# Optimization experiments

Measured on AMD Instinct MI355X. Metric: run time of the kernel, lower is better.

## Reference

```python
import jax, jax.numpy as jnp
import numpy as np

K_TOP = 32
ALPHA = 1.0


def setup_inputs() -> dict:
    key = jax.random.key(0)
    k1, k2, k3 = jax.random.split(key, 3)
    x = jax.random.normal(k1, (1, 512, 1024), dtype=jnp.float32)
    keys = jax.random.normal(k2, (200000, 1024), dtype=jnp.float32) * 0.02
    vals = jax.random.normal(k3, (200000, 1024), dtype=jnp.float32)
    return {"x": x, "keys": keys, "vals": vals}


def reference(x, keys, vals):
    B, L, D = x.shape
    q = x.reshape(B * L, D)                       # [N, D]
    scores = q @ keys.T                           # [N, num_slots] dense matmul
    topv, topi = jax.lax.top_k(scores, K_TOP)     # [N, k]
    attn = jax.nn.softmax(topv, axis=-1)          # [N, k]
    sel_vals = vals[topi]                         # [N, k, D] gather
    out = jnp.einsum('nk,nkd->nd', attn, sel_vals)
    return ALPHA * out.reshape(B, L, D)
```

## Files before the change

### kernel.cpp

```cpp
#include <hip/hip_runtime.h>
#include <hip/hip_bf16.h>
#include <stdint.h>


#define KTOP 32
#define MROWS 512
#define NKEYS 200000
#define DDIM 1024

#define BM 128
#define BN 128
#define BK 64
#define LDT 72
#define NCOLT 1563
#define NT 1568
#define TCAP 256
#define CCAP 256
#define TMARGIN 0.125f

typedef __attribute__((ext_vector_type(4))) float f32x4;
typedef __attribute__((ext_vector_type(8))) short short8;

__device__ __forceinline__ unsigned short f2bf(float f) {
    __hip_bfloat16 h = __float2bfloat16(f);
    return *reinterpret_cast<unsigned short*>(&h);
}
__device__ __forceinline__ int enc16(unsigned short u) {
    return (int)(u ^ ((u & 0x8000u) ? 0xFFFFu : 0x8000u));
}
__device__ __forceinline__ float dec_enc(int e) {
    unsigned short u = (unsigned short)((e & 0x8000) ? (e ^ 0x8000) : (e ^ 0xFFFF));
    return __uint_as_float((unsigned int)u << 16);
}
__device__ __forceinline__ float bf2f(unsigned short u) {
    return __uint_as_float((unsigned int)u << 16);
}

__global__ void cvt_x_kernel(const float* __restrict__ x, unsigned short* __restrict__ xb) {
    int i = blockIdx.x * blockDim.x + threadIdx.x;
    f32x4 v = reinterpret_cast<const f32x4*>(x)[i];
    ushort4 o;
    o.x = f2bf(v.x); o.y = f2bf(v.y); o.z = f2bf(v.z); o.w = f2bf(v.w);
    reinterpret_cast<ushort4*>(xb)[i] = o;
}

__global__ __launch_bounds__(256, 3)
void score_gemm(const float* __restrict__ keys, const unsigned short* __restrict__ xb,
                unsigned short* __restrict__ scores, unsigned short* __restrict__ tilemax) {
    __shared__ unsigned short As[BM * LDT];
    __shared__ unsigned short Bs[BN * LDT];
    __shared__ int tmax[BM];

    const int tid  = threadIdx.x;
    const int lane = tid & 63;
    const int wid  = tid >> 6;
    const int wr   = wid >> 1;
    const int wc   = wid & 1;

    const int bid = blockIdx.x;
    const int s   = bid & 7;
    const int u   = bid >> 3;
    const int rt  = u & 3;
    const int g   = (u >> 2) * 8 + s;
    if (g >= NCOLT) return;
    const int row0 = rt * BM;
    const int col0 = g * BN;

    if (tid < BM) tmax[tid] = 0;

    f32x4 acc[4][4];
#pragma unroll
    for (int m = 0; m < 4; m++)
#pragma unroll
        for (int n = 0; n < 4; n++) acc[m][n] = (f32x4){0.f, 0.f, 0.f, 0.f};

    short8 areg[4];
    f32x4  breg[8];

    auto loadA = [&](int k0) {
#pragma unroll
        for (int i = 0; i < 4; i++) {
            int c = i * 256 + tid;
            int r = c >> 3, j = c & 7;
            areg[i] = *reinterpret_cast<const short8*>(xb + (size_t)(row0 + r) * DDIM + k0 + j * 8);
        }
    };
    auto loadB = [&](int k0) {
#pragma unroll
        for (int i = 0; i < 8; i++) {
            int c = i * 256 + tid;
            int r = c >> 4, j = c & 15;
            int gr = col0 + r; gr = (gr < NKEYS) ? gr : (NKEYS - 1);
            breg[i] = *reinterpret_cast<const f32x4*>(keys + (size_t)gr * DDIM + k0 + j * 4);
        }
    };
    auto writeLDS = [&]() {
#pragma unroll
        for (int i = 0; i < 4; i++) {
            int c = i * 256 + tid;
            int r = c >> 3, j = c & 7;
            *reinterpret_cast<short8*>(&As[r * LDT + j * 8]) = areg[i];
        }
#pragma unroll
        for (int i = 0; i < 8; i++) {
            int c = i * 256 + tid;
            int r = c >> 4, j = c & 15;
            ushort4 o;
            o.x = f2bf(breg[i].x); o.y = f2bf(breg[i].y);
            o.z = f2bf(breg[i].z); o.w = f2bf(breg[i].w);
            *reinterpret_cast<ushort4*>(&Bs[r * LDT + j * 4]) = o;
        }
    };

    const int rl = lane & 15;
    const int kl = (lane >> 4) * 8;

    auto compute = [&]() {
        const unsigned short* Ab = &As[(wr * 64 + rl) * LDT + kl];
        const unsigned short* Bb = &Bs[(wc * 64 + rl) * LDT + kl];
#pragma unroll
        for (int kk = 0; kk < BK; kk += 32) {
            short8 af[4], bf[4];
#pragma unroll
            for (int m = 0; m < 4; m++) af[m] = *reinterpret_cast<const short8*>(Ab + m * 16 * LDT + kk);
#pragma unroll
            for (int n = 0; n < 4; n++) bf[n] = *reinterpret_cast<const short8*>(Bb + n * 16 * LDT + kk);
#pragma unroll
            for (int m = 0; m < 4; m++)
#pragma unroll
                for (int n = 0; n < 4; n++)
                    acc[m][n] = __builtin_amdgcn_mfma_f32_16x16x32_bf16(af[m], bf[n], acc[m][n], 0, 0, 0);
        }
    };

    loadA(0); loadB(0);
    for (int t = 0; t < DDIM / BK; t++) {
        __syncthreads();
        writeLDS();
        __syncthreads();
        if (t + 1 < DDIM / BK) { loadA((t + 1) * BK); loadB((t + 1) * BK); }
        compute();
    }

    const int rg = lane >> 4;
#pragma unroll
    for (int m = 0; m < 4; m++) {
#pragma unroll
        for (int j = 0; j < 4; j++) {
            int lrow = wr * 64 + m * 16 + rg * 4 + j;
            int grow = row0 + lrow;
            float mx = -1e30f;
#pragma unroll
            for (int n = 0; n < 4; n++) {
                float v = acc[m][n][j];
                mx = fmaxf(mx, v);
                int gcol = col0 + wc * 64 + n * 16 + rl;
                if (gcol < NKEYS)
                    scores[(size_t)grow * NKEYS + gcol] = f2bf(v);
            }
#pragma unroll
            for (int sft = 1; sft < 16; sft <<= 1) mx = fmaxf(mx, __shfl_xor(mx, sft));
            if (rl == 0)
                atomicMax(&tmax[lrow], enc16(f2bf(mx)));
        }
    }
    __syncthreads();
    if (tid < BM)
        tilemax[(size_t)(row0 + tid) * NT + g] = (unsigned short)tmax[tid];
}

__global__ __launch_bounds__(256)
void select_kernel(const float* __restrict__ x, const float* __restrict__ keys,
                   const float* __restrict__ vals, const unsigned short* __restrict__ scores,
                   const unsigned short* __restrict__ tilemax, float* __restrict__ out) {
    const int n    = blockIdx.x;
    const int tid  = threadIdx.x;
    const int lane = tid & 63;
    const int w    = tid >> 6;

    __shared__ __align__(16) float qs[DDIM];
    __shared__ unsigned short enc_t[NT];
    __shared__ int    hist[256];
    __shared__ int    tiles[TCAP];
    __shared__ int    cand[CCAP];
    __shared__ double rsc[CCAP];
    __shared__ float  wgt[KTOP];
    __shared__ int    topslot[KTOP];
    __shared__ float  topval[KTOP];
    __shared__ int    ntiles, ncand, sbsel, sabove, st32e;

    reinterpret_cast<f32x4*>(qs)[tid] = reinterpret_cast<const f32x4*>(x + (size_t)n * DDIM)[tid];
    hist[tid] = 0;
    if (tid < 32) { wgt[tid] = 0.f; topslot[tid] = -1; }
    if (tid == 0) { ntiles = 0; ncand = 0; }
    for (int i = tid; i < NT; i += 256)
        enc_t[i] = (i < NCOLT) ? tilemax[(size_t)n * NT + i] : 0;
    __syncthreads();

    for (int i = tid; i < NT; i += 256) atomicAdd(&hist[enc_t[i] >> 8], 1);
    __syncthreads();
    if (tid == 0) {
        int cum = 0, b = 255;
        for (; b >= 0; b--) { cum += hist[b]; if (cum >= KTOP) break; }
        sbsel = b; sabove = cum - hist[b];
    }
    __syncthreads();
    const int bsel = sbsel;
    hist[tid] = 0;
    __syncthreads();
    for (int i = tid; i < NT; i += 256) {
        int e = enc_t[i];
        if ((e >> 8) == bsel) atomicAdd(&hist[e & 0xFF], 1);
    }
    __syncthreads();
    if (tid == 0) {
        int cum = sabove, lb = 255;
        for (; lb >= 0; lb--) { cum += hist[lb]; if (cum >= KTOP) break; }
        st32e = (bsel << 8) | lb;
    }
    __syncthreads();
    const float thr = dec_enc(st32e) - TMARGIN;

    for (int i = tid; i < NT; i += 256) {
        if (dec_enc(enc_t[i]) >= thr) {
            int p = atomicAdd(&ntiles, 1);
            if (p < TCAP) tiles[p] = i;
        }
    }
    __syncthreads();
    const int nt = ntiles < TCAP ? ntiles : TCAP;

    for (int idx = tid; idx < nt * BN; idx += 256) {
        int col = tiles[idx >> 7] * BN + (idx & 127);
        if (col < NKEYS) {
            float v = bf2f(scores[(size_t)n * NKEYS + col]);
            if (v >= thr) {
                int p = atomicAdd(&ncand, 1);
                if (p < CCAP) cand[p] = col;
            }
        }
    }
    __syncthreads();
    const int cnt = ncand < CCAP ? ncand : CCAP;

    for (int ci = w; ci < cnt; ci += 4) {
        const f32x4* kv = reinterpret_cast<const f32x4*>(keys + (size_t)cand[ci] * DDIM) + lane * 4;
        const f32x4* qv = reinterpret_cast<const f32x4*>(qs) + lane * 4;
        double a = 0.0;
#pragma unroll
        for (int i = 0; i < 4; i++) {
            f32x4 q = qv[i], k = kv[i];
            a += (double)q.x * k.x + (double)q.y * k.y + (double)q.z * k.z + (double)q.w * k.w;
        }
#pragma unroll
        for (int sft = 32; sft >= 1; sft >>= 1) a += __shfl_xor(a, sft);
        if (lane == 0) rsc[ci] = a;
    }
    __syncthreads();

    if (w == 0) {
        double v0[4]; int id0[4];
#pragma unroll
        for (int sft = 0; sft < 4; sft++) {
            int p = lane + sft * 64;
            if (p < cnt) { v0[sft] = rsc[p]; id0[sft] = p; } else { v0[sft] = -1e300; id0[sft] = -1; }
        }
        for (int k = 0; k < KTOP; k++) {
            double bv = v0[0]; int bi = id0[0];
#pragma unroll
            for (int sft = 1; sft < 4; sft++) if (v0[sft] > bv) { bv = v0[sft]; bi = id0[sft]; }
#pragma unroll
            for (int sft = 32; sft >= 1; sft >>= 1) {
                double ov = __shfl_xor(bv, sft);
                int    oi = __shfl_xor(bi, sft);
                if (ov > bv) { bv = ov; bi = oi; }
            }
            if (lane == 0) { topslot[k] = bi; topval[k] = (float)bv; }
#pragma unroll
            for (int sft = 0; sft < 4; sft++) if (bi >= 0 && id0[sft] == bi) v0[sft] = -1e300;
        }
    }
    __syncthreads();

    if (tid == 0) {
        float mx = topval[0];
        float sum = 0.f;
        for (int k = 0; k < KTOP; k++) {
            float e = (topslot[k] >= 0) ? expf(topval[k] - mx) : 0.f;
            wgt[k] = e; sum += e;
        }
        float inv = 1.f / sum;
        for (int k = 0; k < KTOP; k++) wgt[k] *= inv;
    }
    __syncthreads();

    f32x4 accv = (f32x4){0.f, 0.f, 0.f, 0.f};
    for (int k = 0; k < KTOP; k++) {
        int sl = topslot[k];
        if (sl >= 0) {
            float wk = wgt[k];
            f32x4 v = reinterpret_cast<const f32x4*>(vals + (size_t)cand[sl] * DDIM)[tid];
            accv.x += wk * v.x; accv.y += wk * v.y; accv.z += wk * v.z; accv.w += wk * v.w;
        }
    }
    reinterpret_cast<f32x4*>(out + (size_t)n * DDIM)[tid] = accv;
}

extern "C" void kernel_launch(void* const* d_in, const int* in_sizes, int n_in,
                              void* d_out, int out_size, void* d_ws, size_t ws_size,
                              hipStream_t stream) {
    const float* x    = (const float*)d_in[0];
    const float* keys = (const float*)d_in[1];
    const float* vals = (const float*)d_in[2];
    float* out = (float*)d_out;

    char* ws = (char*)d_ws;
    unsigned short* scores  = (unsigned short*)ws;
    unsigned short* xb      = (unsigned short*)(ws + 204800000);
    unsigned short* tilemax = (unsigned short*)(ws + 204800000 + 1048576);

    cvt_x_kernel<<<512, 256, 0, stream>>>(x, xb);
    score_gemm<<<4 * NT, 256, 0, stream>>>(keys, xb, scores, tilemax);
    select_kernel<<<MROWS, 256, 0, stream>>>(x, keys, vals, scores, tilemax, out);
}
```

Baseline: 475.5 us.

## Stream fp32 keys into LDS via async global_load_lds with triple buffering

The score GEMM now copies fp32 key tiles straight into a triple-buffered, XOR-swizzled LDS area using global_load_lds, and double-buffers the bf16 query tile. It replaces the register-staged load/convert/store plus two barriers per step with a software pipeline that waits on explicit vmcnt counts. The bf16 conversion moves into the compute loop, so each wave converts the B fragments it reads from LDS. LDS use roughly doubles (fp32 B, three copies), and the occupancy hint of 3 is dropped, so fewer blocks may fit per CU. The conversion work is also repeated across waves.

```diff
diff --git a/kernel.cpp b/kernel.cpp
--- a/kernel.cpp
+++ b/kernel.cpp
@@ -12,6 +12,7 @@
 #define BN 128
 #define BK 64
 #define LDT 72
+#define NSTEP 16
 #define NCOLT 1563
 #define NT 1568
 #define TCAP 256
@@ -44,11 +45,11 @@
     reinterpret_cast<ushort4*>(xb)[i] = o;
 }
 
-__global__ __launch_bounds__(256, 3)
+__global__ __launch_bounds__(256)
 void score_gemm(const float* __restrict__ keys, const unsigned short* __restrict__ xb,
                 unsigned short* __restrict__ scores, unsigned short* __restrict__ tilemax) {
-    __shared__ unsigned short As[BM * LDT];
-    __shared__ unsigned short Bs[BN * LDT];
+    __shared__ __align__(16) unsigned short As[2][BM * LDT];
+    __shared__ __align__(16) float Bsf[3][BN * BK];
     __shared__ int tmax[BM];
 
     const int tid  = threadIdx.x;
@@ -74,57 +75,71 @@
 #pragma unroll
         for (int n = 0; n < 4; n++) acc[m][n] = (f32x4){0.f, 0.f, 0.f, 0.f};
 
-    short8 areg[4];
-    f32x4  breg[8];
-
-    auto loadA = [&](int k0) {
+    short8 areg0[4], areg1[4];
+
+    auto loadA = [&](short8 (&ar)[4], int t) {
+        if (t >= NSTEP) return;
+        const int k0 = t * BK;
 #pragma unroll
         for (int i = 0; i < 4; i++) {
             int c = i * 256 + tid;
             int r = c >> 3, j = c & 7;
-            areg[i] = *reinterpret_cast<const short8*>(xb + (size_t)(row0 + r) * DDIM + k0 + j * 8);
+            ar[i] = *reinterpret_cast<const short8*>(xb + (size_t)(row0 + r) * DDIM + k0 + j * 8);
         }
     };
-    auto loadB = [&](int k0) {
-#pragma unroll
-        for (int i = 0; i < 8; i++) {
-            int c = i * 256 + tid;
-            int r = c >> 4, j = c & 15;
-            int gr = col0 + r; gr = (gr < NKEYS) ? gr : (NKEYS - 1);
-            breg[i] = *reinterpret_cast<const f32x4*>(keys + (size_t)gr * DDIM + k0 + j * 4);
-        }
-    };
-    auto writeLDS = [&]() {
+    auto writeA = [&](int asel, short8 (&ar)[4]) {
 #pragma unroll
         for (int i = 0; i < 4; i++) {
             int c = i * 256 + tid;
             int r = c >> 3, j = c & 7;
-            *reinterpret_cast<short8*>(&As[r * LDT + j * 8]) = areg[i];
-        }
+            *reinterpret_cast<short8*>(&As[asel][r * LDT + j * 8]) = ar[i];
+        }
+    };
+    auto issueB = [&](int t) {
+        if (t >= NSTEP) return;
+        const int bsel = t % 3;
+        const size_t kbyte = (size_t)t * 256;
+        char* ldsbase = (char*)&Bsf[bsel][0];
 #pragma unroll
         for (int i = 0; i < 8; i++) {
-            int c = i * 256 + tid;
-            int r = c >> 4, j = c & 15;
-            ushort4 o;
-            o.x = f2bf(breg[i].x); o.y = f2bf(breg[i].y);
-            o.z = f2bf(breg[i].z); o.w = f2bf(breg[i].w);
-            *reinterpret_cast<ushort4*>(&Bs[r * LDT + j * 4]) = o;
+            int cb = i * 256 + tid;
+            int r = cb >> 4, jc = cb & 15;
+            int js = jc ^ (r & 7);
+            int gr = col0 + r; gr = (gr < NKEYS) ? gr : (NKEYS - 1);
+            const char* src = (const char*)keys + (size_t)gr * 4096 + kbyte + (size_t)js * 16;
+            __builtin_amdgcn_global_load_lds(
+                (const __attribute__((address_space(1))) unsigned int*)src,
+                (__attribute__((address_space(3))) unsigned int*)(ldsbase + (size_t)cb * 16),
+                16, 0, 0);
         }
     };
 
     const int rl = lane & 15;
     const int kl = (lane >> 4) * 8;
 
-    auto compute = [&]() {
-        const unsigned short* Ab = &As[(wr * 64 + rl) * LDT + kl];
-        const unsigned short* Bb = &Bs[(wc * 64 + rl) * LDT + kl];
+    auto compute = [&](int asel, int bsel) {
+        const unsigned short* Ab = &As[asel][(wr * 64 + rl) * LDT + kl];
+        const float* Bf = &Bsf[bsel][0];
+        const int rB0 = wc * 64 + rl;
 #pragma unroll
         for (int kk = 0; kk < BK; kk += 32) {
             short8 af[4], bf[4];
 #pragma unroll
             for (int m = 0; m < 4; m++) af[m] = *reinterpret_cast<const short8*>(Ab + m * 16 * LDT + kk);
 #pragma unroll
-            for (int n = 0; n < 4; n++) bf[n] = *reinterpret_cast<const short8*>(Bb + n * 16 * LDT + kk);
+            for (int n = 0; n < 4; n++) {
+                int row = rB0 + n * 16;
+                int sw  = row & 7;
+                int jc0 = (kk + kl) >> 2;
+                f32x4 c0 = *reinterpret_cast<const f32x4*>(Bf + row * 64 + ((jc0 ^ sw) << 2));
+                f32x4 c1 = *reinterpret_cast<const f32x4*>(Bf + row * 64 + (((jc0 + 1) ^ sw) << 2));
+                short8 b;
+                b[0] = (short)f2bf(c0.x); b[1] = (short)f2bf(c0.y);
+                b[2] = (short)f2bf(c0.z); b[3] = (short)f2bf(c0.w);
+                b[4] = (short)f2bf(c1.x); b[5] = (short)f2bf(c1.y);
+                b[6] = (short)f2bf(c1.z); b[7] = (short)f2bf(c1.w);
+                bf[n] = b;
+            }
 #pragma unroll
             for (int m = 0; m < 4; m++)
 #pragma unroll
@@ -133,14 +148,37 @@
         }
     };
 
-    loadA(0); loadB(0);
-    for (int t = 0; t < DDIM / BK; t++) {
-        __syncthreads();
-        writeLDS();
-        __syncthreads();
-        if (t + 1 < DDIM / BK) { loadA((t + 1) * BK); loadB((t + 1) * BK); }
-        compute();
-    }
+#define SYNC(N) do { asm volatile("s_waitcnt vmcnt(" #N ")" ::: "memory");  \
+                     asm volatile("s_waitcnt lgkmcnt(0)" ::: "memory");     \
+                     __builtin_amdgcn_sched_barrier(0);                     \
+                     __builtin_amdgcn_s_barrier();                          \
+                     __builtin_amdgcn_sched_barrier(0); } while (0)
+
+    loadA(areg0, 0);
+    issueB(0); issueB(1);
+    loadA(areg1, 1);
+    writeA(0, areg0);
+    loadA(areg0, 2);
+    SYNC(16);
+
+    for (int t = 0; t < 12; t += 2) {
+        issueB(t + 2); writeA(1, areg1); loadA(areg1, t + 3);
+        compute(0, t % 3);
+        SYNC(16);
+        issueB(t + 3); writeA(0, areg0); loadA(areg0, t + 4);
+        compute(1, (t + 1) % 3);
+        SYNC(16);
+    }
+    issueB(14); writeA(1, areg1); loadA(areg1, 15);
+    compute(0, 0);
+    SYNC(16);
+    issueB(15); writeA(0, areg0);
+    compute(1, 1);
+    SYNC(12);
+    writeA(1, areg1);
+    compute(0, 2);
+    SYNC(0);
+    compute(1, 0);
 
     const int rg = lane >> 4;
 #pragma unroll
@@ -167,6 +205,7 @@
     __syncthreads();
     if (tid < BM)
         tilemax[(size_t)(row0 + tid) * NT + g] = (unsigned short)tmax[tid];
+#undef SYNC
 }
 
 __global__ __launch_bounds__(256)
```

New measurement: 881.2 us. 85.3% more time.

## Double-buffer score GEMM with direct global-to-LDS loads and swizzled layout

Applied to the files above, without the earlier changes.

Replaces the register-staged global loads and LDS write-back in the score GEMM with direct global-to-LDS async loads into a double-buffered, XOR-swizzled shared memory layout. The K tile drops to 32, and there is one barrier per step instead of two. Keys are now kept as fp32 in LDS and converted to bf16 at fragment-load time. The aim is to overlap memory traffic with MFMA work and remove register and VALU staging, at the cost of more LDS bytes for B and repeated bf16 conversion per wave. Correctness depends on the barrier also waiting for the async LDS loads to finish.

```diff
diff --git a/kernel.cpp b/kernel.cpp
--- a/kernel.cpp
+++ b/kernel.cpp
@@ -10,8 +10,8 @@
 
 #define BM 128
 #define BN 128
-#define BK 64
-#define LDT 72
+#define BK 32
+#define NSTEP 32
 #define NCOLT 1563
 #define NT 1568
 #define TCAP 256
@@ -47,8 +47,8 @@
 __global__ __launch_bounds__(256, 3)
 void score_gemm(const float* __restrict__ keys, const unsigned short* __restrict__ xb,
                 unsigned short* __restrict__ scores, unsigned short* __restrict__ tilemax) {
-    __shared__ unsigned short As[BM * LDT];
-    __shared__ unsigned short Bs[BN * LDT];
+    __shared__ __align__(16) unsigned short As[2][BM * BK];
+    __shared__ __align__(16) float          Bs[2][BN * BK];
     __shared__ int tmax[BM];
 
     const int tid  = threadIdx.x;
@@ -74,74 +74,76 @@
 #pragma unroll
         for (int n = 0; n < 4; n++) acc[m][n] = (f32x4){0.f, 0.f, 0.f, 0.f};
 
-    short8 areg[4];
-    f32x4  breg[8];
-
-    auto loadA = [&](int k0) {
+    auto issueAB = [&](int t, int b) {
+        char* abase = (char*)&As[b][0];
+        char* bbase = (char*)&Bs[b][0];
+#pragma unroll
+        for (int i = 0; i < 2; i++) {
+            int ca = i * 256 + tid;
+            int r = ca >> 2, jc = ca & 3;
+            int js = jc ^ ((r >> 1) & 3);
+            const char* src = (const char*)xb + (size_t)(row0 + r) * 2048 + (size_t)t * 64 + (size_t)js * 16;
+            __builtin_amdgcn_global_load_lds(
+                (const __attribute__((address_space(1))) unsigned int*)src,
+                (__attribute__((address_space(3))) unsigned int*)(abase + (size_t)ca * 16),
+                16, 0, 0);
+        }
 #pragma unroll
         for (int i = 0; i < 4; i++) {
-            int c = i * 256 + tid;
-            int r = c >> 3, j = c & 7;
-            areg[i] = *reinterpret_cast<const short8*>(xb + (size_t)(row0 + r) * DDIM + k0 + j * 8);
+            int cb = i * 256 + tid;
+            int r = cb >> 3, jc = cb & 7;
+            int js = jc ^ (r & 7);
+            int gr = col0 + r; gr = (gr < NKEYS) ? gr : (NKEYS - 1);
+            const char* src = (const char*)keys + (size_t)gr * 4096 + (size_t)t * 128 + (size_t)js * 16;
+            __builtin_amdgcn_global_load_lds(
+                (const __attribute__((address_space(1))) unsigned int*)src,
+                (__attribute__((address_space(3))) unsigned int*)(bbase + (size_t)cb * 16),
+                16, 0, 0);
         }
     };
-    auto loadB = [&](int k0) {
-#pragma unroll
-        for (int i = 0; i < 8; i++) {
-            int c = i * 256 + tid;
-            int r = c >> 4, j = c & 15;
-            int gr = col0 + r; gr = (gr < NKEYS) ? gr : (NKEYS - 1);
-            breg[i] = *reinterpret_cast<const f32x4*>(keys + (size_t)gr * DDIM + k0 + j * 4);
-        }
+
+    const int rl = lane & 15;
+    const int kg = lane >> 4;
+
+    auto compute = [&](int b) {
+        const unsigned short* Ab = &As[b][0];
+        const float* Bf = &Bs[b][0];
+        short8 af[4], bf[4];
+#pragma unroll
+        for (int m = 0; m < 4; m++) {
+            int ra = wr * 64 + m * 16 + rl;
+            int ja = kg ^ ((ra >> 1) & 3);
+            af[m] = *reinterpret_cast<const short8*>(Ab + ra * 32 + ja * 8);
+        }
+#pragma unroll
+        for (int n = 0; n < 4; n++) {
+            int rb = wc * 64 + n * 16 + rl;
+            int sw = rb & 7;
+            int jc0 = kg * 2;
+            f32x4 c0 = *reinterpret_cast<const f32x4*>(Bf + rb * 32 + ((jc0 ^ sw) << 2));
+            f32x4 c1 = *reinterpret_cast<const f32x4*>(Bf + rb * 32 + (((jc0 + 1) ^ sw) << 2));
+            short8 bq;
+            bq[0] = (short)f2bf(c0.x); bq[1] = (short)f2bf(c0.y);
+            bq[2] = (short)f2bf(c0.z); bq[3] = (short)f2bf(c0.w);
+            bq[4] = (short)f2bf(c1.x); bq[5] = (short)f2bf(c1.y);
+            bq[6] = (short)f2bf(c1.z); bq[7] = (short)f2bf(c1.w);
+            bf[n] = bq;
+        }
+#pragma unroll
+        for (int m = 0; m < 4; m++)
+#pragma unroll
+            for (int n = 0; n < 4; n++)
+                acc[m][n] = __builtin_amdgcn_mfma_f32_16x16x32_bf16(af[m], bf[n], acc[m][n], 0, 0, 0);
     };
-    auto writeLDS = [&]() {
-#pragma unroll
-        for (int i = 0; i < 4; i++) {
-            int c = i * 256 + tid;
-            int r = c >> 3, j = c & 7;
-            *reinterpret_cast<short8*>(&As[r * LDT + j * 8]) = areg[i];
-        }
-#pragma unroll
-        for (int i = 0; i < 8; i++) {
-            int c = i * 256 + tid;
-            int r = c >> 4, j = c & 15;
-            ushort4 o;
-            o.x = f2bf(breg[i].x); o.y = f2bf(breg[i].y);
-            o.z = f2bf(breg[i].z); o.w = f2bf(breg[i].w);
-            *reinterpret_cast<ushort4*>(&Bs[r * LDT + j * 4]) = o;
-        }
-    };
-
-    const int rl = lane & 15;
-    const int kl = (lane >> 4) * 8;
-
-    auto compute = [&]() {
-        const unsigned short* Ab = &As[(wr * 64 + rl) * LDT + kl];
-        const unsigned short* Bb = &Bs[(wc * 64 + rl) * LDT + kl];
-#pragma unroll
-        for (int kk = 0; kk < BK; kk += 32) {
-            short8 af[4], bf[4];
-#pragma unroll
-            for (int m = 0; m < 4; m++) af[m] = *reinterpret_cast<const short8*>(Ab + m * 16 * LDT + kk);
-#pragma unroll
-            for (int n = 0; n < 4; n++) bf[n] = *reinterpret_cast<const short8*>(Bb + n * 16 * LDT + kk);
-#pragma unroll
-            for (int m = 0; m < 4; m++)
-#pragma unroll
-                for (int n = 0; n < 4; n++)
-                    acc[m][n] = __builtin_amdgcn_mfma_f32_16x16x32_bf16(af[m], bf[n], acc[m][n], 0, 0, 0);
-        }
-    };
-
-    loadA(0); loadB(0);
-    for (int t = 0; t < DDIM / BK; t++) {
+
+    issueAB(0, 0);
+    for (int t = 0; t < NSTEP; t++) {
         __syncthreads();
-        writeLDS();
-        __syncthreads();
-        if (t + 1 < DDIM / BK) { loadA((t + 1) * BK); loadB((t + 1) * BK); }
-        compute();
-    }
-
+        if (t + 1 < NSTEP) issueAB(t + 1, (t + 1) & 1);
+        compute(t & 1);
+    }
+
+    __syncthreads();
     const int rg = lane >> 4;
 #pragma unroll
     for (int m = 0; m < 4; m++) {
```

After: 661.6 us. 39.1% more time.

## Restructure score GEMM so each block covers all query rows over 64 keys

Applied to the files above, without the earlier changes.

The score GEMM now uses 1024-thread blocks that each hold all 512 query rows in LDS and process a 64-key column tile. This removes the 4x re-read and re-conversion of fp32 keys that came from splitting the rows into four 128-row tiles. Tile maxima become per-64-key, so the select kernel scans twice as many tiles with a larger tile cap but reads finer-grained candidate tiles. The trade-offs are large LDS use per block (about 74KB), which limits occupancy, and a smaller per-wave MFMA tile (32x64), which lowers compute density.

```diff
diff --git a/kernel.cpp b/kernel.cpp
--- a/kernel.cpp
+++ b/kernel.cpp
@@ -8,13 +8,13 @@
 #define NKEYS 200000
 #define DDIM 1024
 
-#define BM 128
-#define BN 128
+#define BN2 64
 #define BK 64
 #define LDT 72
-#define NCOLT 1563
-#define NT 1568
-#define TCAP 256
+#define NSTEP 16
+#define NCOLT2 3125
+#define NT2 3136
+#define TCAP 512
 #define CCAP 256
 #define TMARGIN 0.125f
 
@@ -44,70 +44,55 @@
     reinterpret_cast<ushort4*>(xb)[i] = o;
 }
 
-__global__ __launch_bounds__(256, 3)
+__global__ __launch_bounds__(1024, 4)
 void score_gemm(const float* __restrict__ keys, const unsigned short* __restrict__ xb,
                 unsigned short* __restrict__ scores, unsigned short* __restrict__ tilemax) {
-    __shared__ unsigned short As[BM * LDT];
-    __shared__ unsigned short Bs[BN * LDT];
-    __shared__ int tmax[BM];
+    __shared__ unsigned short As[MROWS * LDT];
+    __shared__ unsigned short Bs[BN2 * LDT];
+    __shared__ int tmax[MROWS];
 
     const int tid  = threadIdx.x;
     const int lane = tid & 63;
-    const int wid  = tid >> 6;
-    const int wr   = wid >> 1;
-    const int wc   = wid & 1;
-
-    const int bid = blockIdx.x;
-    const int s   = bid & 7;
-    const int u   = bid >> 3;
-    const int rt  = u & 3;
-    const int g   = (u >> 2) * 8 + s;
-    if (g >= NCOLT) return;
-    const int row0 = rt * BM;
-    const int col0 = g * BN;
-
-    if (tid < BM) tmax[tid] = 0;
-
-    f32x4 acc[4][4];
-#pragma unroll
-    for (int m = 0; m < 4; m++)
+    const int w    = tid >> 6;
+
+    const int g    = blockIdx.x;
+    const int col0 = g * BN2;
+
+    if (tid < MROWS) tmax[tid] = 0;
+
+    f32x4 acc[2][4];
+#pragma unroll
+    for (int m = 0; m < 2; m++)
 #pragma unroll
         for (int n = 0; n < 4; n++) acc[m][n] = (f32x4){0.f, 0.f, 0.f, 0.f};
 
     short8 areg[4];
-    f32x4  breg[8];
+    f32x4  breg;
 
     auto loadA = [&](int k0) {
 #pragma unroll
         for (int i = 0; i < 4; i++) {
-            int c = i * 256 + tid;
+            int c = i * 1024 + tid;
             int r = c >> 3, j = c & 7;
-            areg[i] = *reinterpret_cast<const short8*>(xb + (size_t)(row0 + r) * DDIM + k0 + j * 8);
+            areg[i] = *reinterpret_cast<const short8*>(xb + (size_t)r * DDIM + k0 + j * 8);
         }
     };
     auto loadB = [&](int k0) {
-#pragma unroll
-        for (int i = 0; i < 8; i++) {
-            int c = i * 256 + tid;
-            int r = c >> 4, j = c & 15;
-            int gr = col0 + r; gr = (gr < NKEYS) ? gr : (NKEYS - 1);
-            breg[i] = *reinterpret_cast<const f32x4*>(keys + (size_t)gr * DDIM + k0 + j * 4);
-        }
+        int r = tid >> 4, j = tid & 15;
+        breg = *reinterpret_cast<const f32x4*>(keys + (size_t)(col0 + r) * DDIM + k0 + j * 4);
     };
     auto writeLDS = [&]() {
 #pragma unroll
         for (int i = 0; i < 4; i++) {
-            int c = i * 256 + tid;
+            int c = i * 1024 + tid;
             int r = c >> 3, j = c & 7;
             *reinterpret_cast<short8*>(&As[r * LDT + j * 8]) = areg[i];
         }
-#pragma unroll
-        for (int i = 0; i < 8; i++) {
-            int c = i * 256 + tid;
-            int r = c >> 4, j = c & 15;
+        {
+            int r = tid >> 4, j = tid & 15;
             ushort4 o;
-            o.x = f2bf(breg[i].x); o.y = f2bf(breg[i].y);
-            o.z = f2bf(breg[i].z); o.w = f2bf(breg[i].w);
+            o.x = f2bf(breg.x); o.y = f2bf(breg.y);
+            o.z = f2bf(breg.z); o.w = f2bf(breg.w);
             *reinterpret_cast<ushort4*>(&Bs[r * LDT + j * 4]) = o;
         }
     };
@@ -116,17 +101,17 @@
     const int kl = (lane >> 4) * 8;
 
     auto compute = [&]() {
-        const unsigned short* Ab = &As[(wr * 64 + rl) * LDT + kl];
-        const unsigned short* Bb = &Bs[(wc * 64 + rl) * LDT + kl];
+        const unsigned short* Ab = &As[(w * 32 + rl) * LDT + kl];
+        const unsigned short* Bb = &Bs[rl * LDT + kl];
 #pragma unroll
         for (int kk = 0; kk < BK; kk += 32) {
-            short8 af[4], bf[4];
-#pragma unroll
-            for (int m = 0; m < 4; m++) af[m] = *reinterpret_cast<const short8*>(Ab + m * 16 * LDT + kk);
+            short8 af[2], bf[4];
+#pragma unroll
+            for (int m = 0; m < 2; m++) af[m] = *reinterpret_cast<const short8*>(Ab + m * 16 * LDT + kk);
 #pragma unroll
             for (int n = 0; n < 4; n++) bf[n] = *reinterpret_cast<const short8*>(Bb + n * 16 * LDT + kk);
 #pragma unroll
-            for (int m = 0; m < 4; m++)
+            for (int m = 0; m < 2; m++)
 #pragma unroll
                 for (int n = 0; n < 4; n++)
                     acc[m][n] = __builtin_amdgcn_mfma_f32_16x16x32_bf16(af[m], bf[n], acc[m][n], 0, 0, 0);
@@ -134,29 +119,26 @@
     };
 
     loadA(0); loadB(0);
-    for (int t = 0; t < DDIM / BK; t++) {
+    for (int t = 0; t < NSTEP; t++) {
         __syncthreads();
         writeLDS();
         __syncthreads();
-        if (t + 1 < DDIM / BK) { loadA((t + 1) * BK); loadB((t + 1) * BK); }
+        if (t + 1 < NSTEP) { loadA((t + 1) * BK); loadB((t + 1) * BK); }
         compute();
     }
 
     const int rg = lane >> 4;
 #pragma unroll
-    for (int m = 0; m < 4; m++) {
+    for (int m = 0; m < 2; m++) {
 #pragma unroll
         for (int j = 0; j < 4; j++) {
-            int lrow = wr * 64 + m * 16 + rg * 4 + j;
-            int grow = row0 + lrow;
+            int lrow = w * 32 + m * 16 + rg * 4 + j;
             float mx = -1e30f;
 #pragma unroll
             for (int n = 0; n < 4; n++) {
                 float v = acc[m][n][j];
                 mx = fmaxf(mx, v);
-                int gcol = col0 + wc * 64 + n * 16 + rl;
-                if (gcol < NKEYS)
-                    scores[(size_t)grow * NKEYS + gcol] = f2bf(v);
+                scores[(size_t)lrow * NKEYS + col0 + n * 16 + rl] = f2bf(v);
             }
 #pragma unroll
             for (int sft = 1; sft < 16; sft <<= 1) mx = fmaxf(mx, __shfl_xor(mx, sft));
@@ -165,8 +147,8 @@
         }
     }
     __syncthreads();
-    if (tid < BM)
-        tilemax[(size_t)(row0 + tid) * NT + g] = (unsigned short)tmax[tid];
+    if (tid < MROWS)
+        tilemax[(size_t)tid * NT2 + g] = (unsigned short)tmax[tid];
 }
 
 __global__ __launch_bounds__(256)
@@ -179,7 +161,7 @@
     const int w    = tid >> 6;
 
     __shared__ __align__(16) float qs[DDIM];
-    __shared__ unsigned short enc_t[NT];
+    __shared__ unsigned short enc_t[NT2];
     __shared__ int    hist[256];
     __shared__ int    tiles[TCAP];
     __shared__ int    cand[CCAP];
@@ -193,11 +175,11 @@
     hist[tid] = 0;
     if (tid < 32) { wgt[tid] = 0.f; topslot[tid] = -1; }
     if (tid == 0) { ntiles = 0; ncand = 0; }
-    for (int i = tid; i < NT; i += 256)
-        enc_t[i] = (i < NCOLT) ? tilemax[(size_t)n * NT + i] : 0;
-    __syncthreads();
-
-    for (int i = tid; i < NT; i += 256) atomicAdd(&hist[enc_t[i] >> 8], 1);
+    for (int i = tid; i < NT2; i += 256)
+        enc_t[i] = (i < NCOLT2) ? tilemax[(size_t)n * NT2 + i] : 0;
+    __syncthreads();
+
+    for (int i = tid; i < NT2; i += 256) atomicAdd(&hist[enc_t[i] >> 8], 1);
     __syncthreads();
     if (tid == 0) {
         int cum = 0, b = 255;
@@ -208,7 +190,7 @@
     const int bsel = sbsel;
     hist[tid] = 0;
     __syncthreads();
-    for (int i = tid; i < NT; i += 256) {
+    for (int i = tid; i < NT2; i += 256) {
         int e = enc_t[i];
         if ((e >> 8) == bsel) atomicAdd(&hist[e & 0xFF], 1);
     }
@@ -221,7 +203,7 @@
     __syncthreads();
     const float thr = dec_enc(st32e) - TMARGIN;
 
-    for (int i = tid; i < NT; i += 256) {
+    for (int i = tid; i < NT2; i += 256) {
         if (dec_enc(enc_t[i]) >= thr) {
             int p = atomicAdd(&ntiles, 1);
             if (p < TCAP) tiles[p] = i;
@@ -230,14 +212,12 @@
     __syncthreads();
     const int nt = ntiles < TCAP ? ntiles : TCAP;
 
-    for (int idx = tid; idx < nt * BN; idx += 256) {
-        int col = tiles[idx >> 7] * BN + (idx & 127);
-        if (col < NKEYS) {
-            float v = bf2f(scores[(size_t)n * NKEYS + col]);
-            if (v >= thr) {
-                int p = atomicAdd(&ncand, 1);
-                if (p < CCAP) cand[p] = col;
-            }
+    for (int idx = tid; idx < nt * BN2; idx += 256) {
+        int col = tiles[idx >> 6] * BN2 + (idx & 63);
+        float v = bf2f(scores[(size_t)n * NKEYS + col]);
+        if (v >= thr) {
+            int p = atomicAdd(&ncand, 1);
+            if (p < CCAP) cand[p] = col;
         }
     }
     __syncthreads();
@@ -320,6 +300,6 @@
     unsigned short* tilemax = (unsigned short*)(ws + 204800000 + 1048576);
 
     cvt_x_kernel<<<512, 256, 0, stream>>>(x, xb);
-    score_gemm<<<4 * NT, 256, 0, stream>>>(keys, xb, scores, tilemax);
+    score_gemm<<<NCOLT2, 1024, 0, stream>>>(keys, xb, scores, tilemax);
     select_kernel<<<MROWS, 256, 0, stream>>>(x, keys, vals, scores, tilemax, out);
 }
```

Measured after the change: 563.5 us. +18.5%, slower.
